# Kernel tuning notes

Measured on AMD Instinct MI355X. Metric: run time of the kernel, lower is better.

## Reference

```python
import jax, jax.numpy as jnp
from jax import lax
import numpy as np

# --- constants matching harris_laplace_detector_batch defaults ---
NUM_OCTAVES = 6
INITIAL_SIGMA = 1.4
HARRIS_K = 0.04
THRESHOLD = 0.01

SOBEL_X = jnp.array([[-1., 0., 1.], [-2., 0., 2.], [-1., 0., 1.]], jnp.float32)
SOBEL_Y = SOBEL_X.T
# OpenCV Laplacian kernel for ksize=3
LAP3 = jnp.array([[2., 0., 2.], [0., -8., 0.], [2., 0., 2.]], jnp.float32)


def _conv2d(x, k):
    """Cross-correlate x [N,H,W] with kernel k [kh,kw], reflect-101 padding (cv2 default)."""
    kh, kw = k.shape
    pt, pb = kh // 2, kh - 1 - kh // 2
    pl, pr = kw // 2, kw - 1 - kw // 2
    xp = jnp.pad(x, ((0, 0), (pt, pb), (pl, pr)), mode='reflect')
    out = lax.conv_general_dilated(xp[:, None], k[None, None], (1, 1), 'VALID')
    return out[:, 0]


def _gaussian_blur(x, sigma):
    """Separable Gaussian blur, truncated at ~3 sigma (static kernel size per octave)."""
    r = max(1, int(3.0 * sigma + 0.5))
    t = jnp.arange(-r, r + 1, dtype=jnp.float32)
    g = jnp.exp(-0.5 * (t / sigma) ** 2)
    g = g / g.sum()
    x = _conv2d(x, g[None, :])  # blur rows
    x = _conv2d(x, g[:, None])  # blur cols
    return x


def setup_inputs() -> dict:
    key = jax.random.key(0)
    images = jax.random.uniform(key, (16, 3, 512, 512), dtype=jnp.float32)
    return {"images": images}


def reference(images) -> jnp.ndarray:
    B, C, H, W = images.shape
    x = images.reshape(B * C, H, W)  # treat each channel independently, as the torch loop does

    # cv2.normalize(..., 0, 255, NORM_MINMAX) per channel (continuous analogue of uint8 cast)
    mn = x.min(axis=(1, 2), keepdims=True)
    mx = x.max(axis=(1, 2), keepdims=True)
    gray = (x - mn) / (mx - mn + 1e-12) * 255.0

    # Harris response: Sobel gradients (ksize=3), 2x2 unnormalized box sum (blockSize=2)
    Ix = _conv2d(gray, SOBEL_X)
    Iy = _conv2d(gray, SOBEL_Y)
    box = jnp.ones((2, 2), jnp.float32)
    Sxx = _conv2d(Ix * Ix, box)
    Syy = _conv2d(Iy * Iy, box)
    Sxy = _conv2d(Ix * Iy, box)
    R = Sxx * Syy - Sxy * Sxy - HARRIS_K * (Sxx + Syy) ** 2

    # cv2.dilate with default 3x3 kernel = 3x3 max filter
    Rd = lax.reduce_window(R, -jnp.inf, lax.max, (1, 3, 3), (1, 1, 1), 'SAME')
    mask = (Rd > THRESHOLD * Rd.max(axis=(1, 2), keepdims=True)).astype(jnp.float32)

    # multi-octave |scaled Laplacian| blurred at each sigma, max-combined
    lap_base = _conv2d(gray, LAP3)
    combined = jnp.zeros_like(gray)
    for octave in range(NUM_OCTAVES):
        sigma = INITIAL_SIGMA * (2.0 ** octave)
        lap = jnp.abs(_gaussian_blur(lap_base * sigma, sigma))
        combined = jnp.maximum(combined, mask * lap)

    # max over channels (the torch loop keeps running np.maximum across channels)
    corners = combined.reshape(B, C, H, W).max(axis=1, keepdims=True)  # [B,1,H,W]
    return corners
```

## Files before the change

### kernel.cpp

```cpp
#include <hip/hip_runtime.h>

#define W 512
#define NPX (512*512)
#define NCH 48
#define NBATCH 16

__device__ __forceinline__ int refl(int i) {
    int a = i < 0 ? -i : i;
    int b = 1022 - a;
    return a < b ? a : b;
}
__device__ __forceinline__ unsigned encf(float f) {
    unsigned u = __float_as_uint(f);
    return (u & 0x80000000u) ? ~u : (u | 0x80000000u);
}
__device__ __forceinline__ float decf(unsigned e) {
    unsigned u = (e & 0x80000000u) ? (e & 0x7FFFFFFFu) : ~e;
    return __uint_as_float(u);
}
__device__ __forceinline__ unsigned long long enc64(double d) {
    unsigned long long u = (unsigned long long)__double_as_longlong(d);
    return (u & 0x8000000000000000ULL) ? ~u : (u | 0x8000000000000000ULL);
}
__device__ __forceinline__ double dec64(unsigned long long e) {
    unsigned long long u = (e & 0x8000000000000000ULL) ? (e & 0x7FFFFFFFFFFFFFFFULL) : ~e;
    return __longlong_as_double((long long)u);
}

__global__ void initK(unsigned* minenc, unsigned* maxenc, unsigned long long* rmaxenc) {
    int t = threadIdx.x;
    if (t < NCH) { minenc[t] = 0xFFFFFFFFu; maxenc[t] = 0u; rmaxenc[t] = 0ULL; }
}

__global__ void gaussK(float* gw) {
    int o = blockIdx.x;
    const int rr[6] = {4, 8, 17, 34, 67, 134};
    int r = rr[o];
    float sigma = 1.4f * (float)(1 << o);
    int t = threadIdx.x;
    int n = 2*r + 1;
    float wv = 0.f;
    if (t < n) { float ft = (float)(t - r) / sigma; wv = expf(-0.5f * ft * ft); }
    __shared__ float red[512];
    red[t] = wv; __syncthreads();
    for (int s = 256; s > 0; s >>= 1) { if (t < s) red[t] += red[t + s]; __syncthreads(); }
    float sum = red[0];
    float* g = gw + o*288;
    if (t < 288) g[t] = (t < n) ? wv / sum : 0.f;
}

__global__ void minmaxK(const float4* __restrict__ x4, unsigned* minenc, unsigned* maxenc) {
    int ch = blockIdx.y, chunk = blockIdx.x, t = threadIdx.x;
    size_t base = (size_t)ch*(NPX/4) + (size_t)chunk*8192;
    float mn = 3.4e38f, mx = -3.4e38f;
    for (int i = t; i < 8192; i += 256) {
        float4 v = x4[base + i];
        mn = fminf(mn, fminf(fminf(v.x, v.y), fminf(v.z, v.w)));
        mx = fmaxf(mx, fmaxf(fmaxf(v.x, v.y), fmaxf(v.z, v.w)));
    }
    for (int o = 32; o; o >>= 1) { mn = fminf(mn, __shfl_down(mn, o)); mx = fmaxf(mx, __shfl_down(mx, o)); }
    __shared__ float smn[4], smx[4];
    if ((t & 63) == 0) { smn[t >> 6] = mn; smx[t >> 6] = mx; }
    __syncthreads();
    if (t == 0) {
        for (int i = 1; i < 4; i++) { mn = fminf(mn, smn[i]); mx = fmaxf(mx, smx[i]); }
        atomicMin(&minenc[ch], encf(mn));
        atomicMax(&maxenc[ch], encf(mx));
    }
}

__global__ void scaleK(const unsigned* minenc, const unsigned* maxenc, double* gsd) {
    int t = threadIdx.x;
    if (t >= NCH) return;
    double mn = (double)decf(minenc[t]), mx = (double)decf(maxenc[t]);
    gsd[t] = 255.0 / (mx - mn + 1e-12);
}

__global__ __launch_bounds__(256) void lapRK(const float* __restrict__ x, const double* __restrict__ gsd,
                      float* __restrict__ lap, double* __restrict__ Rb,
                      unsigned long long* __restrict__ rmaxenc) {
    __shared__ float in[36*36];
    __shared__ double Pxx[33*34], Pyy[33*34], Pxy[33*34];
    int ch = blockIdx.z;
    int px0 = blockIdx.x * 32, py0 = blockIdx.y * 32;
    const float* s = x + (size_t)ch*NPX;
    int t = threadIdx.x;
    for (int i = t; i < 36*36; i += 256) {
        int yy = i / 36, xx = i - yy*36;
        in[i] = s[(size_t)refl(py0 - 2 + yy)*W + refl(px0 - 2 + xx)];
    }
    __syncthreads();
    for (int i = t; i < 33*33; i += 256) {
        int ly = i / 33, lx = i - ly*33;
        const float* c = &in[(ly+1)*36 + (lx+1)];
        double v00 = c[-37], v01 = c[-36], v02 = c[-35];
        double v10 = c[-1],                v12 = c[1];
        double v20 = c[35],  v21 = c[36],  v22 = c[37];
        double ix = (v02 - v00) + 2.0*(v12 - v10) + (v22 - v20);
        double iy = (v20 - v00) + 2.0*(v21 - v01) + (v22 - v02);
        Pxx[ly*34+lx] = ix*ix; Pyy[ly*34+lx] = iy*iy; Pxy[ly*34+lx] = ix*iy;
    }
    __syncthreads();
    double sd = gsd[ch], s2 = sd*sd;
    int tx = t & 31, ty0 = (t >> 5) * 4;
    double m = -1e308;
    #pragma unroll
    for (int q = 0; q < 4; q++) {
        int ly = ty0 + q;
        int gy = py0 + ly, gx = px0 + tx;
        int ya = (gy ? gy-1 : 1) - py0 + 1;
        int yb = ly + 1;
        int xa = (gx ? gx-1 : 1) - px0 + 1;
        int xb = tx + 1;
        double Sxx = (Pxx[ya*34+xa] + Pxx[ya*34+xb]) + (Pxx[yb*34+xa] + Pxx[yb*34+xb]);
        double Syy = (Pyy[ya*34+xa] + Pyy[ya*34+xb]) + (Pyy[yb*34+xa] + Pyy[yb*34+xb]);
        double Sxy = (Pxy[ya*34+xa] + Pxy[ya*34+xb]) + (Pxy[yb*34+xa] + Pxy[yb*34+xb]);
        Sxx *= s2; Syy *= s2; Sxy *= s2;
        double tr = Sxx + Syy;
        double R = Sxx*Syy - Sxy*Sxy - 0.04*tr*tr;
        Rb[(size_t)ch*NPX + (size_t)gy*W + gx] = R;
        const float* c = &in[(ly+2)*36 + (tx+2)];
        double l = 2.0*((double)c[-37] + (double)c[-35] + (double)c[35] + (double)c[37]) - 8.0*(double)c[0];
        lap[(size_t)ch*NPX + (size_t)gy*W + gx] = (float)(sd * l);
        m = fmax(m, R);
    }
    for (int o = 32; o; o >>= 1) m = fmax(m, __shfl_down(m, o));
    __shared__ double sred[4];
    if ((t & 63) == 0) sred[t >> 6] = m;
    __syncthreads();
    if (t == 0) {
        for (int i = 1; i < 4; i++) m = fmax(m, sred[i]);
        atomicMax(&rmaxenc[ch], enc64(m));
    }
}

__global__ __launch_bounds__(256) void maskTK(const double* __restrict__ Rb,
                                              const unsigned long long* __restrict__ rmaxenc,
                                              unsigned char* __restrict__ maskb) {
    __shared__ int bt[34*34];
    int ch = blockIdx.z;
    int px0 = blockIdx.x*32, py0 = blockIdx.y*32;
    double thr = 0.01 * dec64(rmaxenc[ch]);
    const double* R = Rb + (size_t)ch*NPX;
    int t = threadIdx.x;
    for (int i = t; i < 34*34; i += 256) {
        int yy = i / 34, xx = i - yy*34;
        int gy = py0 - 1 + yy, gx = px0 - 1 + xx;
        int v = 0;
        if ((unsigned)gy < 512u && (unsigned)gx < 512u) v = (R[(size_t)gy*W + gx] > thr) ? 1 : 0;
        bt[i] = v;
    }
    __syncthreads();
    int tx = t & 31, ty0 = (t >> 5) * 4;
    #pragma unroll
    for (int q = 0; q < 4; q++) {
        int ly = ty0 + q;
        int c = (ly+1)*34 + tx + 1;
        int v = bt[c-35] | bt[c-34] | bt[c-33] | bt[c-1] | bt[c] | bt[c+1] | bt[c+33] | bt[c+34] | bt[c+35];
        maskb[(size_t)ch*NPX + (size_t)(py0+ly)*W + px0 + tx] = (unsigned char)v;
    }
}

__global__ __launch_bounds__(256) void rowblurK(const float* __restrict__ src, float* __restrict__ dst,
                                                const float* __restrict__ gwo, int r, int nc2) {
    __shared__ float ES[8][16][50];
    __shared__ float wl[288];
    int ch = blockIdx.y;
    int row0 = blockIdx.x * 8;
    int t = threadIdx.x;
    int lr = t >> 5, xi = t & 31;
    for (int i = t; i < 288; i += 256) wl[i] = gwo[i];
    const float* s = src + (size_t)ch*NPX + (size_t)(row0 + lr)*W;
    int n = W + 2*r;
    for (int j = xi; j < 800; j += 32) {
        float v = (j < n) ? s[refl(j - r)] : 0.f;
        ES[lr][j & 15][j >> 4] = v;
    }
    __syncthreads();
    float a[16];
    #pragma unroll
    for (int m = 0; m < 16; m++) a[m] = 0.f;
    for (int cc = 0; cc < nc2; ++cc) {
        float wv[16], f[31];
        #pragma unroll
        for (int i = 0; i < 16; i++) wv[i] = wl[16*cc + i];
        #pragma unroll
        for (int j = 0; j < 31; j++) f[j] = ES[lr][j & 15][xi + cc + (j >> 4)];
        #pragma unroll
        for (int m = 0; m < 16; m++) {
            #pragma unroll
            for (int i = 0; i < 16; i++) a[m] = fmaf(wv[i], f[m + i], a[m]);
        }
    }
    float4* d4 = (float4*)(dst + (size_t)ch*NPX + (size_t)(row0 + lr)*W + xi*16);
    d4[0] = make_float4(a[0],  a[1],  a[2],  a[3]);
    d4[1] = make_float4(a[4],  a[5],  a[6],  a[7]);
    d4[2] = make_float4(a[8],  a[9],  a[10], a[11]);
    d4[3] = make_float4(a[12], a[13], a[14], a[15]);
}

__global__ __launch_bounds__(256) void colblurK(const float* __restrict__ T, const unsigned char* __restrict__ maskb,
                                                float* __restrict__ out, const float* __restrict__ gwo,
                                                int r, int nc2, int rowsAlloc, float sigma, int write0) {
    extern __shared__ float tile[];
    __shared__ float wl[288];
    int x0 = blockIdx.x * 32;
    int band0 = blockIdx.y * 128;
    int b = blockIdx.z;
    int t = threadIdx.x;
    int tx = t & 31, ys = t >> 5;
    int j0 = ys * 16;
    int rowsData = 128 + 2*r;
    for (int i = t; i < 288; i += 256) wl[i] = gwo[i];
    float vm[16];
    #pragma unroll
    for (int m = 0; m < 16; m++) vm[m] = 0.f;
    for (int c = 0; c < 3; ++c) {
        int ch = b*3 + c;
        __syncthreads();
        const float* src = T + (size_t)ch*NPX;
        int tot = rowsAlloc * 32;
        for (int i = t; i < tot; i += 256) {
            int ly = i >> 5, x = i & 31;
            tile[i] = (ly < rowsData) ? src[(size_t)refl(band0 - r + ly)*W + x0 + x] : 0.f;
        }
        __syncthreads();
        const unsigned char* mrow = maskb + (size_t)ch*NPX + (size_t)(band0 + j0)*W + x0 + tx;
        unsigned mkbits = 0;
        #pragma unroll
        for (int m = 0; m < 16; m++) mkbits |= (mrow[(size_t)m*W] ? 1u : 0u) << m;
        unsigned long long bal = __ballot(mkbits != 0);
        bool act = ((bal >> (t & 32)) & 0xFFFFFFFFull) != 0;
        if (act) {
            float a[16];
            #pragma unroll
            for (int m = 0; m < 16; m++) a[m] = 0.f;
            const float* tb = tile + j0*32 + tx;
            for (int cc = 0; cc < nc2; ++cc) {
                float wv[16], f[31];
                #pragma unroll
                for (int i = 0; i < 16; i++) wv[i] = wl[16*cc + i];
                const float* tc = tb + 16*cc*32;
                #pragma unroll
                for (int j = 0; j < 31; j++) f[j] = tc[j * 32];
                #pragma unroll
                for (int m = 0; m < 16; m++) {
                    #pragma unroll
                    for (int i = 0; i < 16; i++) a[m] = fmaf(wv[i], f[m + i], a[m]);
                }
            }
            #pragma unroll
            for (int m = 0; m < 16; m++)
                if (mkbits & (1u << m)) vm[m] = fmaxf(vm[m], sigma * fabsf(a[m]));
        }
    }
    float* ob = out + (size_t)b*NPX + (size_t)(band0 + j0)*W + x0 + tx;
    #pragma unroll
    for (int m = 0; m < 16; m++) {
        float v = vm[m];
        if (!write0) v = fmaxf(v, ob[(size_t)m*W]);
        ob[(size_t)m*W] = v;
    }
}

extern "C" void kernel_launch(void* const* d_in, const int* in_sizes, int n_in,
                              void* d_out, int out_size, void* d_ws, size_t ws_size,
                              hipStream_t stream) {
    const float* x = (const float*)d_in[0];
    float* out = (float*)d_out;
    char* w = (char*)d_ws;
    unsigned* minenc           = (unsigned*)(w + 1024);
    unsigned* maxenc           = (unsigned*)(w + 1280);
    unsigned long long* rmaxenc= (unsigned long long*)(w + 1536);
    double*  gsd               = (double*)(w + 256);
    float*   gw                = (float*)(w + 2048);
    float*   lap               = (float*)(w + 16384);
    double*  Rb                = (double*)(w + 16384 + 50331648);
    float*   T                 = (float*)Rb;
    unsigned char* maskb       = (unsigned char*)(w + 16384 + 50331648 + 100663296);

    initK<<<1, 64, 0, stream>>>(minenc, maxenc, rmaxenc);
    gaussK<<<6, 512, 0, stream>>>(gw);
    minmaxK<<<dim3(8, 48), 256, 0, stream>>>((const float4*)x, minenc, maxenc);
    scaleK<<<1, 64, 0, stream>>>(minenc, maxenc, gsd);
    lapRK<<<dim3(16, 16, 48), 256, 0, stream>>>(x, gsd, lap, Rb, rmaxenc);
    maskTK<<<dim3(16, 16, 48), 256, 0, stream>>>(Rb, rmaxenc, maskb);

    const int rr[6] = {4, 8, 17, 34, 67, 134};
    for (int o = 0; o < 6; ++o) {
        int r = rr[o];
        int nc2 = (2*r + 1 + 15) / 16;
        float sigma = 1.4f * (float)(1 << o);
        rowblurK<<<dim3(64, 48), 256, 0, stream>>>(lap, T, gw + o*288, r, nc2);
        int rowsAlloc = 16*nc2 + 128;
        size_t lds = (size_t)rowsAlloc * 32 * 4;
        colblurK<<<dim3(16, 4, 16), 256, lds, stream>>>(T, maskb, out, gw + o*288, r, nc2, rowsAlloc, sigma, o == 0 ? 1 : 0);
    }
}
```

Measured before the change: 831.6 us.

## Retile column blur into 4-wide float4 threads with templated chunk sizes

The column-blur kernel is rewritten so each thread handles a 4-column by RPT-row patch using float4 LDS loads and padded (36-float) row stride. It is templated on rows-per-thread and tap-chunk size, using finer 8-tap chunks for small radii to cut wasted zero-weight FMAs and a larger band for the widest octave. Mask checks are vectorised and the early-out now uses a wave-wide any. The row-blur LDS arrays are trimmed slightly. This trades more register pressure and different occupancy hints for fewer padded FMAs and wider memory access.

```diff
diff --git a/kernel.cpp b/kernel.cpp
--- a/kernel.cpp
+++ b/kernel.cpp
@@ -163,16 +163,16 @@
 
 __global__ __launch_bounds__(256) void rowblurK(const float* __restrict__ src, float* __restrict__ dst,
                                                 const float* __restrict__ gwo, int r, int nc2) {
-    __shared__ float ES[8][16][50];
-    __shared__ float wl[288];
+    __shared__ float ES[8][16][49];
+    __shared__ float wl[272];
     int ch = blockIdx.y;
     int row0 = blockIdx.x * 8;
     int t = threadIdx.x;
     int lr = t >> 5, xi = t & 31;
-    for (int i = t; i < 288; i += 256) wl[i] = gwo[i];
+    for (int i = t; i < 272; i += 256) wl[i] = gwo[i];
     const float* s = src + (size_t)ch*NPX + (size_t)(row0 + lr)*W;
     int n = W + 2*r;
-    for (int j = xi; j < 800; j += 32) {
+    for (int j = xi; j < 784; j += 32) {
         float v = (j < n) ? s[refl(j - r)] : 0.f;
         ES[lr][j & 15][j >> 4] = v;
     }
@@ -199,67 +199,88 @@
     d4[3] = make_float4(a[12], a[13], a[14], a[15]);
 }
 
-__global__ __launch_bounds__(256) void colblurK(const float* __restrict__ T, const unsigned char* __restrict__ maskb,
-                                                float* __restrict__ out, const float* __restrict__ gwo,
-                                                int r, int nc2, int rowsAlloc, float sigma, int write0) {
-    extern __shared__ float tile[];
-    __shared__ float wl[288];
+template<int RPT, int CHUNK>
+__global__ __launch_bounds__(256, (RPT == 4) ? 4 : 2)
+void colblurK(const float* __restrict__ T, const unsigned char* __restrict__ maskb,
+              float* __restrict__ out, const float* __restrict__ gwo,
+              int r, int nchunk, int rowsAlloc, float sigma, int write0) {
+    extern __shared__ __align__(16) float tile[];
+    float* wl = tile + rowsAlloc*36;
+    const int BAND = RPT*32;
     int x0 = blockIdx.x * 32;
-    int band0 = blockIdx.y * 128;
+    int band0 = blockIdx.y * BAND;
     int b = blockIdx.z;
     int t = threadIdx.x;
-    int tx = t & 31, ys = t >> 5;
-    int j0 = ys * 16;
-    int rowsData = 128 + 2*r;
+    int cg = t & 7, rg = t >> 3;
+    int j0 = rg * RPT;
+    int rowsData = BAND + 2*r;
     for (int i = t; i < 288; i += 256) wl[i] = gwo[i];
-    float vm[16];
-    #pragma unroll
-    for (int m = 0; m < 16; m++) vm[m] = 0.f;
+    float4 vm[RPT];
+    #pragma unroll
+    for (int m = 0; m < RPT; m++) vm[m] = make_float4(0.f, 0.f, 0.f, 0.f);
     for (int c = 0; c < 3; ++c) {
         int ch = b*3 + c;
         __syncthreads();
         const float* src = T + (size_t)ch*NPX;
-        int tot = rowsAlloc * 32;
-        for (int i = t; i < tot; i += 256) {
-            int ly = i >> 5, x = i & 31;
-            tile[i] = (ly < rowsData) ? src[(size_t)refl(band0 - r + ly)*W + x0 + x] : 0.f;
+        for (int ly = rg; ly < rowsAlloc; ly += 32) {
+            float4 v = make_float4(0.f, 0.f, 0.f, 0.f);
+            if (ly < rowsData) v = *(const float4*)(src + (size_t)refl(band0 - r + ly)*W + x0 + 4*cg);
+            *(float4*)(tile + ly*36 + 4*cg) = v;
         }
         __syncthreads();
-        const unsigned char* mrow = maskb + (size_t)ch*NPX + (size_t)(band0 + j0)*W + x0 + tx;
-        unsigned mkbits = 0;
+        const unsigned char* mp = maskb + (size_t)ch*NPX + (size_t)(band0 + j0)*W + x0 + 4*cg;
+        unsigned mk = 0;
         #pragma unroll
-        for (int m = 0; m < 16; m++) mkbits |= (mrow[(size_t)m*W] ? 1u : 0u) << m;
-        unsigned long long bal = __ballot(mkbits != 0);
-        bool act = ((bal >> (t & 32)) & 0xFFFFFFFFull) != 0;
-        if (act) {
-            float a[16];
+        for (int m = 0; m < RPT; m++) {
+            uchar4 u = *(const uchar4*)(mp + (size_t)m*W);
+            mk |= ((u.x ? 1u : 0u) | (u.y ? 2u : 0u) | (u.z ? 4u : 0u) | (u.w ? 8u : 0u)) << (4*m);
+        }
+        if (__any((int)(mk != 0))) {
+            float4 a[RPT];
             #pragma unroll
-            for (int m = 0; m < 16; m++) a[m] = 0.f;
-            const float* tb = tile + j0*32 + tx;
-            for (int cc = 0; cc < nc2; ++cc) {
-                float wv[16], f[31];
+            for (int m = 0; m < RPT; m++) a[m] = make_float4(0.f, 0.f, 0.f, 0.f);
+            const float* tb = tile + j0*36 + 4*cg;
+            for (int cc = 0; cc < nchunk; ++cc) {
+                const float* tc = tb + CHUNK*cc*36;
+                float4 f[RPT + CHUNK - 1];
                 #pragma unroll
-                for (int i = 0; i < 16; i++) wv[i] = wl[16*cc + i];
-                const float* tc = tb + 16*cc*32;
+                for (int j = 0; j < RPT + CHUNK - 1; j++) f[j] = *(const float4*)(tc + j*36);
+                float wv[CHUNK];
                 #pragma unroll
-                for (int j = 0; j < 31; j++) f[j] = tc[j * 32];
+                for (int q = 0; q < CHUNK/4; q++) {
+                    float4 w4 = *(const float4*)(wl + CHUNK*cc + 4*q);
+                    wv[4*q] = w4.x; wv[4*q+1] = w4.y; wv[4*q+2] = w4.z; wv[4*q+3] = w4.w;
+                }
                 #pragma unroll
-                for (int m = 0; m < 16; m++) {
+                for (int m = 0; m < RPT; m++) {
                     #pragma unroll
-                    for (int i = 0; i < 16; i++) a[m] = fmaf(wv[i], f[m + i], a[m]);
+                    for (int i = 0; i < CHUNK; i++) {
+                        a[m].x = fmaf(wv[i], f[m+i].x, a[m].x);
+                        a[m].y = fmaf(wv[i], f[m+i].y, a[m].y);
+                        a[m].z = fmaf(wv[i], f[m+i].z, a[m].z);
+                        a[m].w = fmaf(wv[i], f[m+i].w, a[m].w);
+                    }
                 }
             }
             #pragma unroll
-            for (int m = 0; m < 16; m++)
-                if (mkbits & (1u << m)) vm[m] = fmaxf(vm[m], sigma * fabsf(a[m]));
-        }
-    }
-    float* ob = out + (size_t)b*NPX + (size_t)(band0 + j0)*W + x0 + tx;
-    #pragma unroll
-    for (int m = 0; m < 16; m++) {
-        float v = vm[m];
-        if (!write0) v = fmaxf(v, ob[(size_t)m*W]);
-        ob[(size_t)m*W] = v;
+            for (int m = 0; m < RPT; m++) {
+                if (mk & (1u << (4*m+0))) vm[m].x = fmaxf(vm[m].x, sigma*fabsf(a[m].x));
+                if (mk & (1u << (4*m+1))) vm[m].y = fmaxf(vm[m].y, sigma*fabsf(a[m].y));
+                if (mk & (1u << (4*m+2))) vm[m].z = fmaxf(vm[m].z, sigma*fabsf(a[m].z));
+                if (mk & (1u << (4*m+3))) vm[m].w = fmaxf(vm[m].w, sigma*fabsf(a[m].w));
+            }
+        }
+    }
+    float* ob = out + (size_t)b*NPX + (size_t)(band0 + j0)*W + x0 + 4*cg;
+    #pragma unroll
+    for (int m = 0; m < RPT; m++) {
+        float4 v = vm[m];
+        if (!write0) {
+            float4 cur = *(const float4*)(ob + (size_t)m*W);
+            v.x = fmaxf(v.x, cur.x); v.y = fmaxf(v.y, cur.y);
+            v.z = fmaxf(v.z, cur.z); v.w = fmaxf(v.w, cur.w);
+        }
+        *(float4*)(ob + (size_t)m*W) = v;
     }
 }
 
@@ -289,11 +310,19 @@
     const int rr[6] = {4, 8, 17, 34, 67, 134};
     for (int o = 0; o < 6; ++o) {
         int r = rr[o];
-        int nc2 = (2*r + 1 + 15) / 16;
+        int nc16 = (2*r + 1 + 15) / 16;
         float sigma = 1.4f * (float)(1 << o);
-        rowblurK<<<dim3(64, 48), 256, 0, stream>>>(lap, T, gw + o*288, r, nc2);
-        int rowsAlloc = 16*nc2 + 128;
-        size_t lds = (size_t)rowsAlloc * 32 * 4;
-        colblurK<<<dim3(16, 4, 16), 256, lds, stream>>>(T, maskb, out, gw + o*288, r, nc2, rowsAlloc, sigma, o == 0 ? 1 : 0);
-    }
-}
+        rowblurK<<<dim3(64, 48), 256, 0, stream>>>(lap, T, gw + o*288, r, nc16);
+        if (o == 5) {
+            int nc = nc16;
+            int rowsAlloc = 256 + 16*nc;
+            size_t lds = (size_t)(rowsAlloc*36 + 288) * 4;
+            colblurK<8,16><<<dim3(16, 2, 16), 256, lds, stream>>>(T, maskb, out, gw + o*288, r, nc, rowsAlloc, sigma, 0);
+        } else {
+            int nc = (2*r + 1 + 7) / 8;
+            int rowsAlloc = 128 + 8*nc;
+            size_t lds = (size_t)(rowsAlloc*36 + 288) * 4;
+            colblurK<4,8><<<dim3(16, 4, 16), 256, lds, stream>>>(T, maskb, out, gw + o*288, r, nc, rowsAlloc, sigma, o == 0 ? 1 : 0);
+        }
+    }
+}
```

New measurement: 702.8 us. -15.5%, faster.
